# Optimization experiments

Measured on AMD Instinct MI355X. Metric: run time of the kernel, lower is better.

Reference implementation:

```python
import jax, jax.numpy as jnp
import numpy as np

B, V, C, M, CM, D, OUT = 16, 16, 64, 32, 16, 128, 600
VOCAB = {"cond": 4000, "proc": 2000, "drug": 600, "lab_item": 700, "lab_value": 2000, "inj_item": 400, "inj_value": 2000}


def _gru(x, Wih, Whh, bih, bhh):
    """Batch-first torch-style GRU. x: [N,T,D] -> (outputs [N,T,D], h_T [N,D])."""
    Dh = Whh.shape[1]

    def step(h, xt):
        gi = xt @ Wih.T + bih
        gh = h @ Whh.T + bhh
        ir, iz, ig = jnp.split(gi, 3, axis=-1)
        hr, hz, hg = jnp.split(gh, 3, axis=-1)
        r = jax.nn.sigmoid(ir + hr)
        z = jax.nn.sigmoid(iz + hz)
        n = jnp.tanh(ig + r * hg)
        h = (1.0 - z) * n + z * h
        return h, h

    h0 = jnp.zeros((x.shape[0], Dh), x.dtype)
    hT, ys = jax.lax.scan(step, h0, jnp.swapaxes(x, 0, 1))
    return jnp.swapaxes(ys, 0, 1), hT


def _hetero_mp(feats, Wself, Wmsg):
    """Heterogeneous message passing over node types on the fully-connected
    monitor<->visit-feature bipartite pattern: each node type combines a self
    transform with a transformed mean of the other node types, then ReLU.
    feats: list of [N,D]; Wself/Wmsg: [T,D,D]."""
    stacked = jnp.stack(feats)  # [T,N,D]
    total = jnp.sum(stacked, axis=0)
    T = stacked.shape[0]
    outs = []
    for t in range(T):
        others = (total - stacked[t]) / (T - 1)
        outs.append(jax.nn.relu(stacked[t] @ Wself[t] + others @ Wmsg[t]))
    return outs


def _forward(codes_cond, codes_proc, codes_drug, codes_lab_item, codes_lab_value,
             codes_inj_item, codes_inj_value, weight, age,
             emb_cond, emb_proc, emb_drug, emb_lab_item, emb_lab_value,
             emb_inj_item, emb_inj_value,
             mgru_Wih, mgru_Whh, mgru_bih, mgru_bhh,
             vgru_Wih, vgru_Whh, vgru_bih, vgru_bhh,
             gnn_Wself, gnn_Wmsg,
             fc_weight_W, fc_weight_b, fc_age_W, fc_age_b,
             fc_patient_W, fc_patient_b):
    # ---- visit-event features: embedding lookup + sum-pool over codes ----
    vis = {}
    for k, codes, emb in (("cond", codes_cond, emb_cond),
                          ("proc", codes_proc, emb_proc),
                          ("drug", codes_drug, emb_drug)):
        vis[k] = jnp.sum(emb[codes], axis=2)  # [B,V,D]
    visit_keys = ("cond", "proc", "drug")

    # ---- monitor-event pairs: (item * value) embeddings, GNN, two-level GRU ----
    pairs = (
        (codes_lab_item, codes_lab_value, emb_lab_item, emb_lab_value, "lab_item", (0, 2, 3, 4)),
        (codes_inj_item, codes_inj_value, emb_inj_item, emb_inj_value, "inj_item", (1, 2, 3, 4)),
    )
    hid = {}
    for p, (ci, cv, ei, ev, ikey, gidx) in enumerate(pairs):
        mon = jnp.sum(ei[ci] * ev[cv], axis=3)  # [B,V,M,D]
        feats = [mon.reshape(-1, D)]  # monitor node type, [B*V*M, D]
        for k in visit_keys:  # visit features repeated across monitors
            feats.append(jnp.broadcast_to(vis[k][:, :, None, :], (B, V, M, D)).reshape(-1, D))
        outs = _hetero_mp(feats, gnn_Wself[p], gnn_Wmsg[p])
        for t, k in enumerate((ikey,) + visit_keys):
            g = gidx[t]
            # monitor-level GRU over the M monitors of each visit
            o, _ = _gru(outs[t].reshape(B * V, M, D), mgru_Wih[g], mgru_Whh[g], mgru_bih[g], mgru_bhh[g])
            last = o[:, -1, :].reshape(B, V, D)  # last monitor state per visit
            # visit-level GRU (source uses visit_gru[feature_key1] for all keys)
            _, h = _gru(last, vgru_Wih[p], vgru_Whh[p], vgru_bih[p], vgru_bhh[p])
            hid[k] = h if k not in hid else hid[k] + h

    # ---- weight / age scalar features ----
    for k, x, W, b, vi in (("weight", weight, fc_weight_W, fc_weight_b, 2),
                           ("age", age, fc_age_W, fc_age_b, 3)):
        mask = (x != 0.0)[..., None]  # [B,V,1]
        xe = (x[..., None] * W[:, 0] + b) * mask  # Linear(1->D) then zero-mask
        _, h = _gru(xe, vgru_Wih[vi], vgru_Whh[vi], vgru_bih[vi], vgru_bhh[vi])
        hid[k] = h

    # ---- concat in dict-insertion order, then ReLU + Linear head ----
    pe = jnp.concatenate([hid["lab_item"], hid["cond"], hid["proc"], hid["drug"],
                          hid["inj_item"], hid["weight"], hid["age"]], axis=-1)  # [B, 7D]
    return jax.nn.relu(pe) @ fc_patient_W.T + fc_patient_b  # [B, OUT]


def setup_inputs() -> dict:
    key = jax.random.key(0)
    ks = iter(jax.random.split(key, 64))

    def nrm(shape, s=0.1):
        return (jax.random.normal(next(ks), shape) * s).astype(jnp.float32)

    def emb_table(vsz):
        t = nrm((vsz, D), 1.0)
        return t.at[0].set(0.0)  # padding_idx=0 row is zero

    inp = {}
    inp["codes_cond"] = jax.random.randint(next(ks), (B, V, C), 0, VOCAB["cond"], dtype=jnp.int32)
    inp["codes_proc"] = jax.random.randint(next(ks), (B, V, C), 0, VOCAB["proc"], dtype=jnp.int32)
    inp["codes_drug"] = jax.random.randint(next(ks), (B, V, C), 0, VOCAB["drug"], dtype=jnp.int32)
    inp["codes_lab_item"] = jax.random.randint(next(ks), (B, V, M, CM), 0, VOCAB["lab_item"], dtype=jnp.int32)
    inp["codes_lab_value"] = jax.random.randint(next(ks), (B, V, M, CM), 0, VOCAB["lab_value"], dtype=jnp.int32)
    inp["codes_inj_item"] = jax.random.randint(next(ks), (B, V, M, CM), 0, VOCAB["inj_item"], dtype=jnp.int32)
    inp["codes_inj_value"] = jax.random.randint(next(ks), (B, V, M, CM), 0, VOCAB["inj_value"], dtype=jnp.int32)
    inp["weight"] = jax.random.uniform(next(ks), (B, V), minval=0.1, maxval=1.0, dtype=jnp.float32)
    inp["age"] = jax.random.uniform(next(ks), (B, V), minval=0.1, maxval=1.0, dtype=jnp.float32)
    inp["emb_cond"] = emb_table(VOCAB["cond"])
    inp["emb_proc"] = emb_table(VOCAB["proc"])
    inp["emb_drug"] = emb_table(VOCAB["drug"])
    inp["emb_lab_item"] = emb_table(VOCAB["lab_item"])
    inp["emb_lab_value"] = emb_table(VOCAB["lab_value"])
    inp["emb_inj_item"] = emb_table(VOCAB["inj_item"])
    inp["emb_inj_value"] = emb_table(VOCAB["inj_value"])
    inp["mgru_Wih"] = nrm((5, 3 * D, D))
    inp["mgru_Whh"] = nrm((5, 3 * D, D))
    inp["mgru_bih"] = nrm((5, 3 * D))
    inp["mgru_bhh"] = nrm((5, 3 * D))
    inp["vgru_Wih"] = nrm((4, 3 * D, D))
    inp["vgru_Whh"] = nrm((4, 3 * D, D))
    inp["vgru_bih"] = nrm((4, 3 * D))
    inp["vgru_bhh"] = nrm((4, 3 * D))
    inp["gnn_Wself"] = nrm((2, 4, D, D))
    inp["gnn_Wmsg"] = nrm((2, 4, D, D))
    inp["fc_weight_W"] = nrm((D, 1))
    inp["fc_weight_b"] = nrm((D,))
    inp["fc_age_W"] = nrm((D, 1))
    inp["fc_age_b"] = nrm((D,))
    inp["fc_patient_W"] = nrm((OUT, 7 * D))
    inp["fc_patient_b"] = nrm((OUT,))
    return inp


def reference(codes_cond, codes_proc, codes_drug, codes_lab_item, codes_lab_value,
              codes_inj_item, codes_inj_value, weight, age,
              emb_cond, emb_proc, emb_drug, emb_lab_item, emb_lab_value,
              emb_inj_item, emb_inj_value,
              mgru_Wih, mgru_Whh, mgru_bih, mgru_bhh,
              vgru_Wih, vgru_Whh, vgru_bih, vgru_bhh,
              gnn_Wself, gnn_Wmsg,
              fc_weight_W, fc_weight_b, fc_age_W, fc_age_b,
              fc_patient_W, fc_patient_b):
    return _forward(codes_cond, codes_proc, codes_drug, codes_lab_item, codes_lab_value,
                    codes_inj_item, codes_inj_value, weight, age,
                    emb_cond, emb_proc, emb_drug, emb_lab_item, emb_lab_value,
                    emb_inj_item, emb_inj_value,
                    mgru_Wih, mgru_Whh, mgru_bih, mgru_bhh,
                    vgru_Wih, vgru_Whh, vgru_bih, vgru_bhh,
                    gnn_Wself, gnn_Wmsg,
                    fc_weight_W, fc_weight_b, fc_age_W, fc_age_b,
                    fc_patient_W, fc_patient_b)
```

## Files before the change

kernel.cpp:

```cpp
#include <hip/hip_runtime.h>
#include <math.h>

#define B_   16
#define V_   16
#define C_   64
#define M_   32
#define CM_  16
#define D_   128
#define OUT_ 600
#define NSEQ 256
#define NROW 8192

typedef __attribute__((ext_vector_type(8))) short bf16x8;
typedef __attribute__((ext_vector_type(4))) float f32x4;

__device__ __forceinline__ unsigned short f2bf(float x) {
  union { float f; unsigned u; } v; v.f = x;
  unsigned r = v.u + 0x7fff + ((v.u >> 16) & 1);
  return (unsigned short)(r >> 16);
}
__device__ __forceinline__ float fsig(float x)  { return __fdividef(1.f, 1.f + __expf(-x)); }
__device__ __forceinline__ float ftanh(float x) { return 1.f - 2.f*__fdividef(1.f, __expf(2.f*x) + 1.f); }

constexpr int OFF_VIS   = 0;
constexpr int OFF_VISB  = 98304;
constexpr int OFF_MONB  = 147456;
constexpr int OFF_TOTB  = 1196032;
constexpr int OFF_W12T  = 2244608;
constexpr int OFF_WIHB  = 2375680;
constexpr int OFF_WIHTV = 2498560;
constexpr int OFF_XE    = 2695168;
constexpr int OFF_GI    = 2760704;
constexpr int OFF_LAST  = 27926528;
constexpr int OFF_VGI   = 28188672;
constexpr int OFF_VH    = 29171712;
constexpr int OFF_PE    = 29192192;

__global__ __launch_bounds__(256) void k_prep(
    const float* __restrict__ Wself, const float* __restrict__ Wmsg,
    const float* __restrict__ mWih,  const float* __restrict__ vWih,
    const float* __restrict__ wgt,   const float* __restrict__ age,
    const float* __restrict__ fwW,   const float* __restrict__ fwB,
    const float* __restrict__ faW,   const float* __restrict__ faB,
    short* __restrict__ w12t, short* __restrict__ wihb,
    float* __restrict__ wihTv, float* __restrict__ xe)
{
  int bx = blockIdx.x, tid = threadIdx.x;
  if (bx < 1024) {
    int lin = bx*256 + tid;
    int pt = lin >> 15, rem = lin & 32767;
    int n = rem >> 8, k = rem & 255;
    float v;
    if (k < 128) v = Wself[pt*16384 + k*128 + n] - Wmsg[pt*16384 + k*128 + n]*(1.f/3.f);
    else         v = Wmsg[pt*16384 + (k-128)*128 + n]*(1.f/3.f);
    w12t[lin] = (short)f2bf(v);
  } else if (bx < 1984) {
    int lin = (bx-1024)*256 + tid;
    wihb[lin] = (short)f2bf(mWih[lin]);
  } else if (bx < 2752) {
    int lin = (bx-1984)*256 + tid;
    int g = lin / 49152, rem2 = lin % 49152;
    int k = rem2 / 384, j = rem2 % 384;
    wihTv[lin] = vWih[g*49152 + j*128 + k];
  } else {
    int lin = (bx-2752)*256 + tid;
    int which = lin >> 15, rem2 = lin & 32767;
    int n = rem2 >> 7, d = rem2 & 127;
    float x  = which ? age[n] : wgt[n];
    float Wv = which ? faW[d] : fwW[d];
    float bb = which ? faB[d] : fwB[d];
    xe[lin] = (x != 0.0f) ? (x*Wv + bb) : 0.0f;
  }
}

__global__ __launch_bounds__(128) void k_vis(
    const int* __restrict__ cc, const int* __restrict__ cp, const int* __restrict__ cd,
    const float* __restrict__ ec, const float* __restrict__ ep, const float* __restrict__ ed,
    float* __restrict__ vis, short* __restrict__ visb)
{
  int type = blockIdx.x >> 8;
  int bv   = blockIdx.x & 255;
  int d    = threadIdx.x;
  const int*   codes = (type==0) ? cc : (type==1) ? cp : cd;
  const float* emb   = (type==0) ? ec : (type==1) ? ep : ed;
  float acc = 0.f;
  for (int c = 0; c < C_; ++c) {
    int code = codes[bv*C_ + c];
    acc += emb[code*D_ + d];
  }
  vis [(type*NSEQ + bv)*D_ + d] = acc;
  visb[(type*NSEQ + bv)*D_ + d] = (short)f2bf(acc);
}

__global__ __launch_bounds__(128) void k_mon(
    const int* __restrict__ cli, const int* __restrict__ clv,
    const int* __restrict__ cii, const int* __restrict__ civ,
    const float* __restrict__ eli, const float* __restrict__ elv,
    const float* __restrict__ eii, const float* __restrict__ eiv,
    const float* __restrict__ vis,
    short* __restrict__ monb, short* __restrict__ totb)
{
  int p   = blockIdx.x >> 13;
  int bvm = blockIdx.x & 8191;
  int d   = threadIdx.x;
  const int* ci = p ? cii : cli;  const int* cv = p ? civ : clv;
  const float* ei = p ? eii : eli; const float* ev = p ? eiv : elv;
  float acc = 0.f;
  #pragma unroll
  for (int c = 0; c < CM_; ++c) {
    int iv = ci[bvm*CM_ + c];
    int vv = cv[bvm*CM_ + c];
    acc += ei[iv*D_ + d] * ev[vv*D_ + d];
  }
  int bv = bvm >> 5;
  float vsum = vis[bv*D_ + d] + vis[(NSEQ + bv)*D_ + d] + vis[(2*NSEQ + bv)*D_ + d];
  monb[(p*NROW + bvm)*D_ + d] = (short)f2bf(acc);
  totb[(p*NROW + bvm)*D_ + d] = (short)f2bf(acc + vsum);
}

__global__ __launch_bounds__(256, 2) void k_gg(
    const short* __restrict__ monb, const short* __restrict__ totb,
    const short* __restrict__ visb, const short* __restrict__ w12t,
    const short* __restrict__ wihb, const float* __restrict__ mbih,
    float* __restrict__ gi)
{
  const int pt = blockIdx.x >> 6;
  const int rb = blockIdx.x & 63;
  const int p = pt >> 2, t = pt & 3;
  const int g = (pt % 4 == 0) ? (pt / 4) : (pt % 4 + 1);
  const int row0 = rb * 128;
  const int tid = threadIdx.x;
  const int w = tid >> 6, lane = tid & 63;
  const int c = lane & 15, q = lane >> 4;

  __shared__ short smem[2*128*72];
  short (*Xs)[72]  = (short(*)[72])smem;
  short (*Ws)[72]  = (short(*)[72])(smem + 128*72);
  short (*Ys)[136] = (short(*)[136])smem;
  float (*giS)[68] = (float(*)[68])smem;

  const int rowL = tid >> 1, kc = tid & 1;
  const int rowG = row0 + rowL;
  const int bv = rowG >> 5;
  const int mg = w >> 1, ng = w & 1;

  f32x4 acc1[4][4];
  #pragma unroll
  for (int mi = 0; mi < 4; ++mi)
    #pragma unroll
    for (int ni = 0; ni < 4; ++ni) acc1[mi][ni] = (f32x4){0.f,0.f,0.f,0.f};

  const short* featp = (t == 0) ? (monb + ((size_t)p*NROW + rowG)*128)
                                : (visb + ((size_t)(t-1)*NSEQ + bv)*128);
  const short* totp  = totb + ((size_t)p*NROW + rowG)*128;
  const short* wrow  = w12t + ((size_t)pt*128 + rowL)*256;

  #pragma unroll 1
  for (int ks = 0; ks < 4; ++ks) {
    __syncthreads();
    int kg = ks*64 + kc*32;
    const short* srcX = (kg < 128) ? (featp + kg) : (totp + (kg - 128));
    const short* srcW = wrow + kg;
    short* dX = &Xs[rowL][kc*32];
    short* dW = &Ws[rowL][kc*32];
    #pragma unroll
    for (int i = 0; i < 4; ++i) {
      *(bf16x8*)(dX + 8*i) = *(const bf16x8*)(srcX + 8*i);
      *(bf16x8*)(dW + 8*i) = *(const bf16x8*)(srcW + 8*i);
    }
    __syncthreads();
    #pragma unroll
    for (int kk = 0; kk < 2; ++kk) {
      bf16x8 af[4], bfr[4];
      #pragma unroll
      for (int mi = 0; mi < 4; ++mi)
        af[mi] = *(const bf16x8*)&Xs[(mg*4+mi)*16 + c][kk*32 + q*8];
      #pragma unroll
      for (int ni = 0; ni < 4; ++ni)
        bfr[ni] = *(const bf16x8*)&Ws[(ng*4+ni)*16 + c][kk*32 + q*8];
      #pragma unroll
      for (int mi = 0; mi < 4; ++mi)
        #pragma unroll
        for (int ni = 0; ni < 4; ++ni)
          acc1[mi][ni] = __builtin_amdgcn_mfma_f32_16x16x32_bf16(af[mi], bfr[ni], acc1[mi][ni], 0, 0, 0);
    }
  }
  __syncthreads();

  #pragma unroll
  for (int mi = 0; mi < 4; ++mi)
    #pragma unroll
    for (int ni = 0; ni < 4; ++ni)
      #pragma unroll
      for (int reg = 0; reg < 4; ++reg)
        Ys[(mg*4+mi)*16 + q*4 + reg][(ng*4+ni)*16 + c] =
            (short)f2bf(fmaxf(acc1[mi][ni][reg], 0.f));
  __syncthreads();

  bf16x8 Af[2][4];
  #pragma unroll
  for (int mi = 0; mi < 2; ++mi)
    #pragma unroll
    for (int kt = 0; kt < 4; ++kt)
      Af[mi][kt] = *(const bf16x8*)&Ys[(w*2+mi)*16 + c][kt*32 + q*8];

  float bihv[24];
  #pragma unroll
  for (int nt = 0; nt < 24; ++nt)
    bihv[nt] = mbih[g*384 + nt*16 + c];

  float* gslab = gi + (((size_t)pt*64 + rb)*32)*384*4;
  #pragma unroll 1
  for (int cn = 0; cn < 6; ++cn) {
    f32x4 acc2[2][4];
    #pragma unroll
    for (int mi = 0; mi < 2; ++mi)
      #pragma unroll
      for (int ni = 0; ni < 4; ++ni) acc2[mi][ni] = (f32x4){0.f,0.f,0.f,0.f};
    #pragma unroll
    for (int ni = 0; ni < 4; ++ni) {
      int n = (cn*4 + ni)*16 + c;
      const short* bp_ = wihb + ((size_t)g*384 + n)*128 + q*8;
      #pragma unroll
      for (int kt = 0; kt < 4; ++kt) {
        bf16x8 bfr = *(const bf16x8*)(bp_ + kt*32);
        #pragma unroll
        for (int mi = 0; mi < 2; ++mi)
          acc2[mi][ni] = __builtin_amdgcn_mfma_f32_16x16x32_bf16(Af[mi][kt], bfr, acc2[mi][ni], 0, 0, 0);
      }
    }
    __syncthreads();
    #pragma unroll
    for (int mi = 0; mi < 2; ++mi)
      #pragma unroll
      for (int ni = 0; ni < 4; ++ni) {
        float bia = bihv[cn*4+ni];
        #pragma unroll
        for (int reg = 0; reg < 4; ++reg)
          giS[(w*2+mi)*16 + q*4 + reg][ni*16 + c] = acc2[mi][ni][reg] + bia;
      }
    __syncthreads();
    #pragma unroll
    for (int k = 0; k < 8; ++k) {
      int o4 = tid + k*256;
      int m = o4 >> 6, colL = o4 & 63;
      float4 v = make_float4(giS[m][colL], giS[32+m][colL],
                             giS[64+m][colL], giS[96+m][colL]);
      *(float4*)&gslab[((size_t)m*384 + cn*64 + colL)*4] = v;
    }
  }
}

__global__ __launch_bounds__(512, 1) void k_mgru(
    const float* __restrict__ gi, const float* __restrict__ mWhh,
    const float* __restrict__ mbhh, float* __restrict__ last)
{
  const int run = blockIdx.x >> 5, grp = blockIdx.x & 31;
  const int g = (run % 4 == 0) ? (run / 4) : (run % 4 + 1);
  const int tid = threadIdx.x;
  const int w = tid >> 6;
  const int lane = tid & 63;
  const int c = lane & 15, q = lane >> 4;

  __shared__ short hb[2][4][16][40];
  for (int idx = tid; idx < 2*4*16*40; idx += 512)
    ((short*)hb)[idx] = 0;

  const int jh = w*16 + c;

  bf16x8 bfrag[3][4];
  #pragma unroll
  for (int gate = 0; gate < 3; ++gate) {
    const float* wp = mWhh + ((size_t)g*384 + gate*128 + jh)*128 + q*8;
    #pragma unroll
    for (int kt = 0; kt < 4; ++kt) {
      float4 lo = *(const float4*)(wp + kt*32);
      float4 hi = *(const float4*)(wp + kt*32 + 4);
      bf16x8 t;
      t[0]=(short)f2bf(lo.x); t[1]=(short)f2bf(lo.y); t[2]=(short)f2bf(lo.z); t[3]=(short)f2bf(lo.w);
      t[4]=(short)f2bf(hi.x); t[5]=(short)f2bf(hi.y); t[6]=(short)f2bf(hi.z); t[7]=(short)f2bf(hi.w);
      bfrag[gate][kt] = t;
    }
  }
  float bh_[3];
  #pragma unroll
  for (int gate = 0; gate < 3; ++gate)
    bh_[gate] = mbhh[g*384 + gate*128 + jh];

  float hf[4] = {0.f,0.f,0.f,0.f};
  const float* gib = gi + (((size_t)run*64 + grp*2 + q)*32)*384*4;
  const bool act = (lane < 32);

  f32x4 gA[3], gB[3];
  if (act) {
    #pragma unroll
    for (int gate = 0; gate < 3; ++gate)
      gA[gate] = *(const f32x4*)&gib[(size_t)(0*384 + gate*128 + jh)*4];
  }
  __syncthreads();

  auto dostep = [&](int m, f32x4 (&gcur)[3], f32x4 (&gnext)[3]) {
    const int cur = m & 1, nxt = cur ^ 1;
    bf16x8 a[4];
    #pragma unroll
    for (int kt = 0; kt < 4; ++kt)
      a[kt] = *(const bf16x8*)&hb[cur][kt][c][q*8];

    f32x4 acc[3];
    #pragma unroll
    for (int gate = 0; gate < 3; ++gate) {
      f32x4 t = {0.f,0.f,0.f,0.f};
      #pragma unroll
      for (int kt = 0; kt < 4; ++kt)
        t = __builtin_amdgcn_mfma_f32_16x16x32_bf16(a[kt], bfrag[gate][kt], t, 0, 0, 0);
      acc[gate] = t;
    }

    if (act && m < 31) {
      #pragma unroll
      for (int gate = 0; gate < 3; ++gate)
        gnext[gate] = *(const f32x4*)&gib[(size_t)((m+1)*384 + gate*128 + jh)*4];
    }

    if (act) {
      const int kt = jh >> 5, kk = jh & 31;
      #pragma unroll
      for (int reg = 0; reg < 4; ++reg) {
        int row = q*4 + reg;
        float rr = fsig(acc[0][reg] + bh_[0] + gcur[0][reg]);
        float zz = fsig(acc[1][reg] + bh_[1] + gcur[1][reg]);
        float nn = ftanh(gcur[2][reg] + rr*(acc[2][reg] + bh_[2]));
        float hnew = (1.f - zz)*nn + zz*hf[reg];
        hf[reg] = hnew;
        hb[nxt][kt][row][kk] = (short)f2bf(hnew);
      }
    }
    __syncthreads();
  };

  #pragma unroll 1
  for (int m2 = 0; m2 < 16; ++m2) {
    dostep(2*m2,     gA, gB);
    dostep(2*m2 + 1, gB, gA);
  }

  if (act) {
    #pragma unroll
    for (int reg = 0; reg < 4; ++reg)
      last[(run*NSEQ + grp*8 + q*4 + reg)*D_ + jh] = hf[reg];
  }
}

__global__ __launch_bounds__(384) void k_vgi(
    const float* __restrict__ last, const float* __restrict__ xe,
    const float* __restrict__ wihTv, const float* __restrict__ vbih,
    float* __restrict__ vgi)
{
  int run = blockIdx.x >> 5;
  int rblk = blockIdx.x & 31;
  int j = threadIdx.x;
  int vidx = (run < 4) ? 0 : (run < 8) ? 1 : (run - 6);
  __shared__ float Xs[8][128];
  const float* X = (run < 8) ? (last + run*NSEQ*D_) : (xe + (run-8)*NSEQ*D_);
  for (int idx = j; idx < 1024; idx += 384) {
    int s = idx >> 7, k = idx & 127;
    Xs[s][k] = X[(rblk*8 + s)*D_ + k];
  }
  __syncthreads();
  float acc[8];
  float bias = vbih[vidx*384 + j];
  #pragma unroll
  for (int s = 0; s < 8; ++s) acc[s] = bias;
  const float* W = wihTv + vidx*49152 + j;
  #pragma unroll 4
  for (int k = 0; k < 128; ++k) {
    float wv = W[k*384];
    #pragma unroll
    for (int s = 0; s < 8; ++s) acc[s] += Xs[s][k] * wv;
  }
  #pragma unroll
  for (int s = 0; s < 8; ++s)
    vgi[(run*NSEQ + rblk*8 + s)*384 + j] = acc[s];
}

__global__ __launch_bounds__(768) void k_vgru(
    const float* __restrict__ vgi, const float* __restrict__ vWhh,
    const float* __restrict__ vbhh, float* __restrict__ vh)
{
  int run = blockIdx.x >> 4, b = blockIdx.x & 15;
  int tid = threadIdx.x;
  int j = tid >> 1, kh = tid & 1;
  int vidx = (run < 4) ? 0 : (run < 8) ? 1 : (run - 6);
  float w[64];
  const float4* wrow = (const float4*)(vWhh + (vidx*384 + j)*128 + kh*64);
  #pragma unroll
  for (int k4 = 0; k4 < 16; ++k4) {
    float4 t4 = wrow[k4];
    w[4*k4] = t4.x; w[4*k4+1] = t4.y; w[4*k4+2] = t4.z; w[4*k4+3] = t4.w;
  }
  float bj = vbhh[vidx*384 + j];
  __shared__ __align__(16) float hsv[128];
  __shared__ float gh[384];
  if (tid < 128) hsv[tid] = 0.f;
  __syncthreads();
  const float* gib = vgi + (run*NSEQ + b*16)*384;
  #pragma unroll 1
  for (int v = 0; v < 16; ++v) {
    const float4* h4 = (const float4*)(hsv + kh*64);
    float p0 = 0.f, p1 = 0.f;
    #pragma unroll
    for (int k4 = 0; k4 < 8; ++k4) {
      float4 u0 = h4[k4], u1 = h4[k4+8];
      p0 += w[4*k4   ]*u0.x + w[4*k4+1 ]*u0.y + w[4*k4+2 ]*u0.z + w[4*k4+3 ]*u0.w;
      p1 += w[4*k4+32]*u1.x + w[4*k4+33]*u1.y + w[4*k4+34]*u1.z + w[4*k4+35]*u1.w;
    }
    float part = p0 + p1;
    part += __shfl_xor(part, 1);
    if (kh == 0) gh[j] = bj + ((j < 256) ? gib[v*384 + j] : 0.f) + part;
    __syncthreads();
    if (tid < 128) {
      float r = fsig(gh[tid]);
      float z = fsig(gh[tid+128]);
      float gin = gib[v*384 + 256 + tid];
      float n = ftanh(gin + r*gh[tid+256]);
      hsv[tid] = (1.f - z)*n + z*hsv[tid];
    }
    __syncthreads();
  }
  if (tid < 128) vh[(run*16 + b)*D_ + tid] = hsv[tid];
}

__global__ __launch_bounds__(256) void k_pe(
    const float* __restrict__ vh, float* __restrict__ pe)
{
  int idx = blockIdx.x*256 + threadIdx.x;
  int b = idx / 896, cc2 = idx % 896;
  int s = cc2 >> 7, d = cc2 & 127;
  const int a1[7] = {0,1,2,3,4,8,9};
  const int a2[7] = {-1,5,6,7,-1,-1,-1};
  float v = vh[(a1[s]*16 + b)*D_ + d];
  int s2 = a2[s];
  if (s2 >= 0) v += vh[(s2*16 + b)*D_ + d];
  pe[idx] = fmaxf(v, 0.f);
}

__global__ __launch_bounds__(256) void k_head(
    const float* __restrict__ pe, const float* __restrict__ Wp,
    const float* __restrict__ bp, float* __restrict__ out)
{
  const int o = blockIdx.x;
  const int tid = threadIdx.x;
  const int b = tid & 15, kc = tid >> 4;
  const float4* pb = (const float4*)(pe + b*896 + kc*56);
  const float4* wb = (const float4*)(Wp + (size_t)o*896 + kc*56);
  float acc = 0.f;
  #pragma unroll
  for (int i = 0; i < 14; ++i) {
    float4 a = pb[i], w = wb[i];
    acc += a.x*w.x + a.y*w.y + a.z*w.z + a.w*w.w;
  }
  __shared__ float red[16][17];
  red[kc][b] = acc;
  __syncthreads();
  if (tid < 16) {
    float s = 0.f;
    #pragma unroll
    for (int k = 0; k < 16; ++k) s += red[k][tid];
    out[tid*OUT_ + o] = s + bp[o];
  }
}

extern "C" void kernel_launch(void* const* d_in, const int* in_sizes, int n_in,
                              void* d_out, int out_size, void* d_ws, size_t ws_size,
                              hipStream_t stream)
{
  (void)in_sizes; (void)n_in; (void)out_size; (void)ws_size;
  const int*   cc   = (const int*)  d_in[0];
  const int*   cp   = (const int*)  d_in[1];
  const int*   cd   = (const int*)  d_in[2];
  const int*   cli  = (const int*)  d_in[3];
  const int*   clv  = (const int*)  d_in[4];
  const int*   cii  = (const int*)  d_in[5];
  const int*   civ  = (const int*)  d_in[6];
  const float* wgt  = (const float*)d_in[7];
  const float* age  = (const float*)d_in[8];
  const float* ec   = (const float*)d_in[9];
  const float* ep   = (const float*)d_in[10];
  const float* ed   = (const float*)d_in[11];
  const float* eli  = (const float*)d_in[12];
  const float* elv  = (const float*)d_in[13];
  const float* eii  = (const float*)d_in[14];
  const float* eiv  = (const float*)d_in[15];
  const float* mWih = (const float*)d_in[16];
  const float* mWhh = (const float*)d_in[17];
  const float* mbih = (const float*)d_in[18];
  const float* mbhh = (const float*)d_in[19];
  const float* vWih = (const float*)d_in[20];
  const float* vWhh = (const float*)d_in[21];
  const float* vbih = (const float*)d_in[22];
  const float* vbhh = (const float*)d_in[23];
  const float* Wself= (const float*)d_in[24];
  const float* Wmsg = (const float*)d_in[25];
  const float* fwW  = (const float*)d_in[26];
  const float* fwB  = (const float*)d_in[27];
  const float* faW  = (const float*)d_in[28];
  const float* faB  = (const float*)d_in[29];
  const float* Wp   = (const float*)d_in[30];
  const float* bp   = (const float*)d_in[31];
  float* out = (float*)d_out;
  float* ws  = (float*)d_ws;

  float* vis   = ws + OFF_VIS;
  short* visb  = (short*)(ws + OFF_VISB);
  short* monb  = (short*)(ws + OFF_MONB);
  short* totb  = (short*)(ws + OFF_TOTB);
  short* w12t  = (short*)(ws + OFF_W12T);
  short* wihb  = (short*)(ws + OFF_WIHB);
  float* wihTv = ws + OFF_WIHTV;
  float* xe    = ws + OFF_XE;
  float* gi    = ws + OFF_GI;
  float* last  = ws + OFF_LAST;
  float* vgi   = ws + OFF_VGI;
  float* vh    = ws + OFF_VH;
  float* pe    = ws + OFF_PE;

  k_prep<<<3008, 256, 0, stream>>>(Wself, Wmsg, mWih, vWih, wgt, age,
                                   fwW, fwB, faW, faB, w12t, wihb, wihTv, xe);
  k_vis <<<768, 128, 0, stream>>>(cc, cp, cd, ec, ep, ed, vis, visb);
  k_mon <<<16384, 128, 0, stream>>>(cli, clv, cii, civ, eli, elv, eii, eiv,
                                    vis, monb, totb);
  k_gg  <<<512, 256, 0, stream>>>(monb, totb, visb, w12t, wihb, mbih, gi);
  k_mgru<<<256, 512, 0, stream>>>(gi, mWhh, mbhh, last);
  k_vgi <<<320, 384, 0, stream>>>(last, xe, wihTv, vbih, vgi);
  k_vgru<<<160, 768, 0, stream>>>(vgi, vWhh, vbhh, vh);
  k_pe  <<<56, 256, 0, stream>>>(vh, pe);
  k_head<<<600, 256, 0, stream>>>(pe, Wp, bp, out);
}
```

Measured before the change: 284.6 us.

## Stage monitor GRU input gates through LDS in chunks, allow two blocks per CU

The monitor GRU kernel previously had each active lane prefetch its next step's input-gate values from global memory into registers. Now the block cooperatively loads 4-step chunks of gi into a 48KB shared buffer with coalesced float4 loads, and reads them from LDS during the steps. Launch bounds also change to allow two blocks per CU. The chunk loads are not overlapped with compute, so each chunk adds a global-load stall plus an extra barrier. The larger LDS use and tighter register budget may also limit occupancy or cause spills.

After: 290.3 us. +2.0%, slower.

```diff
diff --git a/kernel.cpp b/kernel.cpp
--- a/kernel.cpp
+++ b/kernel.cpp
@@ -251,7 +251,7 @@
   }
 }
 
-__global__ __launch_bounds__(512, 1) void k_mgru(
+__global__ __launch_bounds__(512, 2) void k_mgru(
     const float* __restrict__ gi, const float* __restrict__ mWhh,
     const float* __restrict__ mbhh, float* __restrict__ last)
 {
@@ -263,6 +263,7 @@
   const int c = lane & 15, q = lane >> 4;
 
   __shared__ short hb[2][4][16][40];
+  __shared__ float giL[12288];
   for (int idx = tid; idx < 2*4*16*40; idx += 512)
     ((short*)hb)[idx] = 0;
 
@@ -288,60 +289,63 @@
     bh_[gate] = mbhh[g*384 + gate*128 + jh];
 
   float hf[4] = {0.f,0.f,0.f,0.f};
-  const float* gib = gi + (((size_t)run*64 + grp*2 + q)*32)*384*4;
+  const float* gslab = gi + (((size_t)run*64 + grp*2)*32)*384*4;
   const bool act = (lane < 32);
-
-  f32x4 gA[3], gB[3];
-  if (act) {
-    #pragma unroll
-    for (int gate = 0; gate < 3; ++gate)
-      gA[gate] = *(const f32x4*)&gib[(size_t)(0*384 + gate*128 + jh)*4];
-  }
   __syncthreads();
 
-  auto dostep = [&](int m, f32x4 (&gcur)[3], f32x4 (&gnext)[3]) {
-    const int cur = m & 1, nxt = cur ^ 1;
-    bf16x8 a[4];
-    #pragma unroll
-    for (int kt = 0; kt < 4; ++kt)
-      a[kt] = *(const bf16x8*)&hb[cur][kt][c][q*8];
-
-    f32x4 acc[3];
-    #pragma unroll
-    for (int gate = 0; gate < 3; ++gate) {
-      f32x4 t = {0.f,0.f,0.f,0.f};
+  #pragma unroll 1
+  for (int chunk = 0; chunk < 8; ++chunk) {
+    float4 tmp[6];
+    #pragma unroll
+    for (int i = 0; i < 6; ++i) {
+      int off = i*2048 + tid*4;
+      int r = (i >= 3);
+      int local = off - r*6144;
+      tmp[i] = *(const float4*)(gslab + (size_t)r*49152 + chunk*6144 + local);
+    }
+    #pragma unroll
+    for (int i = 0; i < 6; ++i)
+      *(float4*)&giL[i*2048 + tid*4] = tmp[i];
+    __syncthreads();
+
+    #pragma unroll 1
+    for (int mm = 0; mm < 4; ++mm) {
+      const int m = chunk*4 + mm;
+      const int cur = m & 1, nxt = cur ^ 1;
+      bf16x8 a[4];
       #pragma unroll
       for (int kt = 0; kt < 4; ++kt)
-        t = __builtin_amdgcn_mfma_f32_16x16x32_bf16(a[kt], bfrag[gate][kt], t, 0, 0, 0);
-      acc[gate] = t;
-    }
-
-    if (act && m < 31) {
-      #pragma unroll
-      for (int gate = 0; gate < 3; ++gate)
-        gnext[gate] = *(const f32x4*)&gib[(size_t)((m+1)*384 + gate*128 + jh)*4];
-    }
-
-    if (act) {
-      const int kt = jh >> 5, kk = jh & 31;
-      #pragma unroll
-      for (int reg = 0; reg < 4; ++reg) {
-        int row = q*4 + reg;
-        float rr = fsig(acc[0][reg] + bh_[0] + gcur[0][reg]);
-        float zz = fsig(acc[1][reg] + bh_[1] + gcur[1][reg]);
-        float nn = ftanh(gcur[2][reg] + rr*(acc[2][reg] + bh_[2]));
-        float hnew = (1.f - zz)*nn + zz*hf[reg];
-        hf[reg] = hnew;
-        hb[nxt][kt][row][kk] = (short)f2bf(hnew);
+        a[kt] = *(const bf16x8*)&hb[cur][kt][c][q*8];
+
+      f32x4 acc[3];
+      #pragma unroll
+      for (int gate = 0; gate < 3; ++gate) {
+        f32x4 t = {0.f,0.f,0.f,0.f};
+        #pragma unroll
+        for (int kt = 0; kt < 4; ++kt)
+          t = __builtin_amdgcn_mfma_f32_16x16x32_bf16(a[kt], bfrag[gate][kt], t, 0, 0, 0);
+        acc[gate] = t;
       }
-    }
-    __syncthreads();
-  };
-
-  #pragma unroll 1
-  for (int m2 = 0; m2 < 16; ++m2) {
-    dostep(2*m2,     gA, gB);
-    dostep(2*m2 + 1, gB, gA);
+
+      if (act) {
+        f32x4 gv[3];
+        #pragma unroll
+        for (int gate = 0; gate < 3; ++gate)
+          gv[gate] = *(const f32x4*)&giL[((q*4 + mm)*384 + gate*128 + jh)*4];
+        const int kt = jh >> 5, kk = jh & 31;
+        #pragma unroll
+        for (int reg = 0; reg < 4; ++reg) {
+          int row = q*4 + reg;
+          float rr = fsig(acc[0][reg] + bh_[0] + gv[0][reg]);
+          float zz = fsig(acc[1][reg] + bh_[1] + gv[1][reg]);
+          float nn = ftanh(gv[2][reg] + rr*(acc[2][reg] + bh_[2]));
+          float hnew = (1.f - zz)*nn + zz*hf[reg];
+          hf[reg] = hnew;
+          hb[nxt][kt][row][kk] = (short)f2bf(hnew);
+        }
+      }
+      __syncthreads();
+    }
   }
 
   if (act) {
```
